# Optimization experiments

Hardware: AMD Instinct MI355X
Metric: run time of the kernel (lower is better)

Reference implementation:

```python
import jax, jax.numpy as jnp
import numpy as np

N, E, C_IN, HID, G, L = 100000, 1600000, 64, 32, 128, 3
NEG_SLOPE = 0.01  # F.leaky_relu default


def setup_inputs() -> dict:
    key = jax.random.key(0)
    ks = jax.random.split(key, 10)
    x = jax.random.normal(ks[0], (N, C_IN), dtype=jnp.float32)
    src = jax.random.randint(ks[1], (E,), 0, N, dtype=jnp.int32)
    dst = jax.random.randint(ks[2], (E,), 0, N, dtype=jnp.int32)
    batch = jnp.sort(jax.random.randint(ks[3], (N,), 0, G, dtype=jnp.int32))
    def glorot(k, fan_in, fan_out):
        lim = np.sqrt(6.0 / (fan_in + fan_out)).astype(np.float32)
        return jax.random.uniform(k, (fan_in, fan_out), jnp.float32, -lim, lim)
    W0 = glorot(ks[4], C_IN, HID); b0 = jnp.zeros((HID,), jnp.float32)
    W1 = glorot(ks[5], HID, HID);  b1 = jnp.zeros((HID,), jnp.float32)
    W2 = glorot(ks[6], HID, HID);  b2 = jnp.zeros((HID,), jnp.float32)
    return {"x": x, "W0": W0, "b0": b0, "W1": W1, "b1": b1,
            "W2": W2, "b2": b2, "src": src, "dst": dst, "batch": batch}


def _gcn_conv(x, W, b, src, dst, dinv):
    # PyG GCNConv: h = x W; aggregate with sym-norm (A + I)
    h = x @ W                                   # [N, H]
    coef = (dinv[src] * dinv[dst])[:, None]     # [E, 1]
    msg = h[src] * coef                         # gather + scale
    agg = jax.ops.segment_sum(msg, dst, num_segments=N)
    agg = agg + h * (dinv * dinv)[:, None]      # self-loop term
    return agg + b


def _mean_pool(x, batch, counts):
    s = jax.ops.segment_sum(x, batch, num_segments=G)
    return s / counts[:, None]


def reference(x, W0, b0, W1, b1, W2, b2, src, dst, batch):
    # degree with self loops (edge weight 1), as PyG gcn_norm does
    deg = jax.ops.segment_sum(jnp.ones((E,), x.dtype), dst, num_segments=N) + 1.0
    dinv = jax.lax.rsqrt(deg)
    counts = jnp.maximum(
        jax.ops.segment_sum(jnp.ones((N,), x.dtype), batch, num_segments=G), 1.0)
    params = [(W0, b0), (W1, b1), (W2, b2)]
    feats = []
    h = x
    for W, b in params:
        h = _gcn_conv(h, W, b, src, dst, dinv)
        h = jax.nn.leaky_relu(h, NEG_SLOPE)
        feats.append(_mean_pool(h, batch, counts))
    merge = jnp.mean(jnp.stack(feats, axis=0), axis=0)  # [G, HID]
    return merge
```

## Files before the change

kernel.cpp:

```cpp
#include <hip/hip_runtime.h>
#include <hip/hip_bf16.h>

#define NN 100000
#define NE 1600000
#define CIN 64
#define HIDN 32
#define NG 128
#define SLOPE 0.01f


__global__ __launch_bounds__(256) void k_rank(const int* __restrict__ dst,
                                              int* __restrict__ deg,
                                              int* __restrict__ rank,
                                              int qbase, int qcount) {
  int i0 = blockIdx.x * 256 + threadIdx.x;
  if (i0 >= qcount) return;
  int i = qbase + i0;
  int4 d = ((const int4*)dst)[i];
  int4 r;
  r.x = atomicAdd(&deg[d.x], 1);
  r.y = atomicAdd(&deg[d.y], 1);
  r.z = atomicAdd(&deg[d.z], 1);
  r.w = atomicAdd(&deg[d.w], 1);
  ((int4*)rank)[i] = r;
}


__global__ __launch_bounds__(256) void k_scan1(const int* __restrict__ deg,
                                               int* __restrict__ bsum) {
  __shared__ int s[256];
  int t = threadIdx.x;
  int base = blockIdx.x * 1024 + t * 4;
  int sum = 0;
#pragma unroll
  for (int j = 0; j < 4; ++j) {
    int idx = base + j;
    if (idx < NN) sum += deg[idx];
  }
  s[t] = sum;
  __syncthreads();
  for (int o = 128; o > 0; o >>= 1) {
    if (t < o) s[t] += s[t + o];
    __syncthreads();
  }
  if (t == 0) bsum[blockIdx.x] = s[0];
}

__global__ __launch_bounds__(256) void k_mid(int* __restrict__ bsum,
                                             int* __restrict__ rowp,
                                             const int* __restrict__ batch,
                                             float* __restrict__ cinv, int nblk) {
  __shared__ int s[128];
  __shared__ int sb[NG + 1];
  int t = threadIdx.x;
  if (t < nblk) s[t] = bsum[t];
  if (t <= NG) {
    int lo = 0, hi = NN;
    while (lo < hi) {
      int mid = (lo + hi) >> 1;
      if (batch[mid] < t) lo = mid + 1; else hi = mid;
    }
    sb[t] = lo;
  }
  __syncthreads();
  if (t == 0) {
    int run = 0;
    for (int i = 0; i < nblk; ++i) {
      int v = s[i];
      s[i] = run;
      run += v;
    }
    rowp[NN] = run;
  }
  __syncthreads();
  if (t < nblk) bsum[t] = s[t];
  if (t < NG) {
    int c = sb[t + 1] - sb[t];
    cinv[t] = 1.0f / (3.0f * fmaxf((float)c, 1.0f));
  }
}

__global__ __launch_bounds__(256) void k_scan3(const int* __restrict__ deg,
                                               const int* __restrict__ bsum,
                                               int* __restrict__ rowp,
                                               float* __restrict__ dinv) {
  __shared__ int s[256];
  int t = threadIdx.x;
  int base = blockIdx.x * 1024 + t * 4;
  int d0 = 0, d1 = 0, d2 = 0, d3 = 0;
  if (base < NN) d0 = deg[base];
  if (base + 1 < NN) d1 = deg[base + 1];
  if (base + 2 < NN) d2 = deg[base + 2];
  if (base + 3 < NN) d3 = deg[base + 3];
  int ts = d0 + d1 + d2 + d3;
  s[t] = ts;
  __syncthreads();
  for (int o = 1; o < 256; o <<= 1) {
    int v = (t >= o) ? s[t - o] : 0;
    __syncthreads();
    s[t] += v;
    __syncthreads();
  }
  int run = bsum[blockIdx.x] + s[t] - ts;
  if (base < NN) { rowp[base] = run; dinv[base] = rsqrtf((float)d0 + 1.0f); run += d0; }
  if (base + 1 < NN) { rowp[base + 1] = run; dinv[base + 1] = rsqrtf((float)d1 + 1.0f); run += d1; }
  if (base + 2 < NN) { rowp[base + 2] = run; dinv[base + 2] = rsqrtf((float)d2 + 1.0f); run += d2; }
  if (base + 3 < NN) { rowp[base + 3] = run; dinv[base + 3] = rsqrtf((float)d3 + 1.0f); run += d3; }
}

__global__ __launch_bounds__(256) void k_scatter(const int* __restrict__ src,
                                                 const int* __restrict__ dst,
                                                 const int* __restrict__ rank,
                                                 const int* __restrict__ rowp,
                                                 int* __restrict__ col,
                                                 int qbase, int qcount) {
  int i0 = blockIdx.x * 256 + threadIdx.x;
  if (i0 >= qcount) return;
  int i = qbase + i0;
  int4 d = ((const int4*)dst)[i];
  int4 r = ((const int4*)rank)[i];
  int4 s = ((const int4*)src)[i];
  col[rowp[d.x] + r.x] = s.x;
  col[rowp[d.y] + r.y] = s.y;
  col[rowp[d.z] + r.z] = s.z;
  col[rowp[d.w] + r.w] = s.w;
}


template <int K>
__global__ __launch_bounds__(256) void k_mm(const float* __restrict__ in,
                                            const float* __restrict__ W,
                                            const float* __restrict__ dinv,
                                            __hip_bfloat16* __restrict__ out) {
  __shared__ float sW[K * HIDN];
  int t = threadIdx.x;
  for (int i = t; i < K * HIDN; i += 256) sW[i] = W[i];
  __syncthreads();
  int gid = blockIdx.x * 256 + t;
  int node = gid >> 5;
  int f = gid & 31;
  if (node >= NN) return;
  const float* xr = in + node * K;
  float acc = 0.f;
#pragma unroll
  for (int k = 0; k < K; ++k) acc += xr[k] * sW[k * HIDN + f];
  out[node * HIDN + f] = __float2bfloat16(acc * dinv[node]);
}


template <int WRITE_H>
__global__ __launch_bounds__(256) void k_agg(const __hip_bfloat16* __restrict__ hs,
                                             const int* __restrict__ rowp,
                                             const int* __restrict__ col,
                                             const float* __restrict__ dinv,
                                             const int* __restrict__ batch,
                                             const float* __restrict__ cinv,
                                             const float* __restrict__ bias,
                                             float* __restrict__ hout,
                                             float* __restrict__ pool) {
  const int t = threadIdx.x;
  const int f = t & 31;
  const int sub = t >> 5;
  const float bf = bias[f];
  float pacc = 0.f;
  int gcur = -1;
  const int base = blockIdx.x * 32;
#pragma unroll
  for (int it = 0; it < 4; ++it) {
    const int i = base + it * 8 + sub;
    if (i < NN) {
      float acc = __bfloat162float(hs[i * HIDN + f]);
      const int rs = rowp[i];
      const int re = rowp[i + 1];
      int e = rs;
      for (; e + 8 <= re; e += 8) {
        const int c0 = __builtin_nontemporal_load(col + e);
        const int c1 = __builtin_nontemporal_load(col + e + 1);
        const int c2 = __builtin_nontemporal_load(col + e + 2);
        const int c3 = __builtin_nontemporal_load(col + e + 3);
        const int c4 = __builtin_nontemporal_load(col + e + 4);
        const int c5 = __builtin_nontemporal_load(col + e + 5);
        const int c6 = __builtin_nontemporal_load(col + e + 6);
        const int c7 = __builtin_nontemporal_load(col + e + 7);
        const float v0 = __bfloat162float(hs[c0 * HIDN + f]);
        const float v1 = __bfloat162float(hs[c1 * HIDN + f]);
        const float v2 = __bfloat162float(hs[c2 * HIDN + f]);
        const float v3 = __bfloat162float(hs[c3 * HIDN + f]);
        const float v4 = __bfloat162float(hs[c4 * HIDN + f]);
        const float v5 = __bfloat162float(hs[c5 * HIDN + f]);
        const float v6 = __bfloat162float(hs[c6 * HIDN + f]);
        const float v7 = __bfloat162float(hs[c7 * HIDN + f]);
        acc += ((v0 + v1) + (v2 + v3)) + ((v4 + v5) + (v6 + v7));
      }
      for (; e + 4 <= re; e += 4) {
        const int c0 = __builtin_nontemporal_load(col + e);
        const int c1 = __builtin_nontemporal_load(col + e + 1);
        const int c2 = __builtin_nontemporal_load(col + e + 2);
        const int c3 = __builtin_nontemporal_load(col + e + 3);
        const float v0 = __bfloat162float(hs[c0 * HIDN + f]);
        const float v1 = __bfloat162float(hs[c1 * HIDN + f]);
        const float v2 = __bfloat162float(hs[c2 * HIDN + f]);
        const float v3 = __bfloat162float(hs[c3 * HIDN + f]);
        acc += (v0 + v1) + (v2 + v3);
      }
      for (; e < re; ++e) acc += __bfloat162float(hs[col[e] * HIDN + f]);
      float v = acc * dinv[i] + bf;
      v = v > 0.f ? v : SLOPE * v;
      if (WRITE_H) hout[i * HIDN + f] = v;
      const int g = batch[i];
      if (g != gcur) {
        if (gcur >= 0) unsafeAtomicAdd(&pool[gcur * HIDN + f], pacc * cinv[gcur]);
        gcur = g;
        pacc = 0.f;
      }
      pacc += v;
    }
  }
  if (gcur >= 0) unsafeAtomicAdd(&pool[gcur * HIDN + f], pacc * cinv[gcur]);
}


extern "C" void kernel_launch(void* const* d_in, const int* in_sizes, int n_in,
                              void* d_out, int out_size, void* d_ws, size_t ws_size,
                              hipStream_t stream) {
  const float* x = (const float*)d_in[0];
  const float* W0 = (const float*)d_in[1];
  const float* b0 = (const float*)d_in[2];
  const float* W1 = (const float*)d_in[3];
  const float* b1 = (const float*)d_in[4];
  const float* W2 = (const float*)d_in[5];
  const float* b2 = (const float*)d_in[6];
  const int* src = (const int*)d_in[7];
  const int* dst = (const int*)d_in[8];
  const int* batch = (const int*)d_in[9];
  float* out = (float*)d_out;

  char* ws = (char*)d_ws;
  auto carve = [&](size_t bytes) -> char* {
    char* p = ws;
    ws += (bytes + 255) & ~(size_t)255;
    return p;
  };
  int* deg = (int*)carve(NN * 4);
  int* rank = (int*)carve((size_t)NE * 4);
  int* rowp = (int*)carve((NN + 1) * 4);
  int* bsum = (int*)carve(128 * 4);
  float* dinv = (float*)carve(NN * 4);
  float* cinv = (float*)carve(NG * 4);
  int* col = (int*)carve((size_t)NE * 4);
  float* hA = (float*)carve((size_t)NN * HIDN * 4);
  __hip_bfloat16* hs = (__hip_bfloat16*)carve((size_t)NN * HIDN * 2);

  hipMemsetAsync(deg, 0, NN * 4, stream);
  hipMemsetAsync(out, 0, NG * HIDN * 4, stream);

  const int QH = NE / 4 / 2;
  const int half_grid = (QH + 255) / 256;
  k_rank<<<half_grid, 256, 0, stream>>>(dst, deg, rank, 0, QH);
  k_rank<<<half_grid, 256, 0, stream>>>(dst, deg, rank, QH, QH);

  int nblk = (NN + 1023) / 1024;
  k_scan1<<<nblk, 256, 0, stream>>>(deg, bsum);
  k_mid<<<1, 256, 0, stream>>>(bsum, rowp, batch, cinv, nblk);
  k_scan3<<<nblk, 256, 0, stream>>>(deg, bsum, rowp, dinv);

  k_scatter<<<half_grid, 256, 0, stream>>>(src, dst, rank, rowp, col, 0, QH);
  k_scatter<<<half_grid, 256, 0, stream>>>(src, dst, rank, rowp, col, QH, QH);

  const int mm_grid = (NN * HIDN + 255) / 256;
  const int agg_grid = (NN + 31) / 32;

  k_mm<CIN><<<mm_grid, 256, 0, stream>>>(x, W0, dinv, hs);
  k_agg<1><<<agg_grid, 256, 0, stream>>>(hs, rowp, col, dinv, batch, cinv, b0, hA, out);
  k_mm<HIDN><<<mm_grid, 256, 0, stream>>>(hA, W1, dinv, hs);
  k_agg<1><<<agg_grid, 256, 0, stream>>>(hs, rowp, col, dinv, batch, cinv, b1, hA, out);
  k_mm<HIDN><<<mm_grid, 256, 0, stream>>>(hA, W2, dinv, hs);
  k_agg<0><<<agg_grid, 256, 0, stream>>>(hs, rowp, col, dinv, batch, cinv, b2, hA, out);
}
```

Baseline: 473.6 us.

## Balance edge work across warps in aggregation and pack edge ranks into bytes

The aggregation kernel now splits each 32-node block's edge range evenly across its 8 warps, not one node per warp. Each warp accumulates per-row partial sums into shared memory with atomics, and the epilogue then applies self-loop, bias, activation and pooling. Edge ranks are packed as 8-bit values, four per word, which cuts rank traffic. The rank and scatter kernels are merged into single launches handling 8 edges per thread, and the output memset is folded into k_mid. The packing assumes every in-degree is below 256, and the grid assumes NN divisible by 32, so both depend on this input shape.

```diff
diff --git a/kernel.cpp b/kernel.cpp
--- a/kernel.cpp
+++ b/kernel.cpp
@@ -11,18 +11,23 @@
 
 __global__ __launch_bounds__(256) void k_rank(const int* __restrict__ dst,
                                               int* __restrict__ deg,
-                                              int* __restrict__ rank,
-                                              int qbase, int qcount) {
-  int i0 = blockIdx.x * 256 + threadIdx.x;
-  if (i0 >= qcount) return;
-  int i = qbase + i0;
-  int4 d = ((const int4*)dst)[i];
-  int4 r;
-  r.x = atomicAdd(&deg[d.x], 1);
-  r.y = atomicAdd(&deg[d.y], 1);
-  r.z = atomicAdd(&deg[d.z], 1);
-  r.w = atomicAdd(&deg[d.w], 1);
-  ((int4*)rank)[i] = r;
+                                              unsigned int* __restrict__ rank) {
+  int i = blockIdx.x * 256 + threadIdx.x;
+  if (i * 8 >= NE) return;
+  int4 a = ((const int4*)dst)[2 * i];
+  int4 b = ((const int4*)dst)[2 * i + 1];
+  unsigned int r0 = atomicAdd(&deg[a.x], 1);
+  unsigned int r1 = atomicAdd(&deg[a.y], 1);
+  unsigned int r2 = atomicAdd(&deg[a.z], 1);
+  unsigned int r3 = atomicAdd(&deg[a.w], 1);
+  unsigned int r4 = atomicAdd(&deg[b.x], 1);
+  unsigned int r5 = atomicAdd(&deg[b.y], 1);
+  unsigned int r6 = atomicAdd(&deg[b.z], 1);
+  unsigned int r7 = atomicAdd(&deg[b.w], 1);
+  uint2 packed;
+  packed.x = r0 | (r1 << 8) | (r2 << 16) | (r3 << 24);
+  packed.y = r4 | (r5 << 8) | (r6 << 16) | (r7 << 24);
+  ((uint2*)rank)[i] = packed;
 }
 
 
@@ -49,7 +54,8 @@
 __global__ __launch_bounds__(256) void k_mid(int* __restrict__ bsum,
                                              int* __restrict__ rowp,
                                              const int* __restrict__ batch,
-                                             float* __restrict__ cinv, int nblk) {
+                                             float* __restrict__ cinv,
+                                             float* __restrict__ out, int nblk) {
   __shared__ int s[128];
   __shared__ int sb[NG + 1];
   int t = threadIdx.x;
@@ -62,6 +68,7 @@
     }
     sb[t] = lo;
   }
+  for (int i = t; i < NG * HIDN; i += 256) out[i] = 0.f;
   __syncthreads();
   if (t == 0) {
     int run = 0;
@@ -110,20 +117,26 @@
 
 __global__ __launch_bounds__(256) void k_scatter(const int* __restrict__ src,
                                                  const int* __restrict__ dst,
-                                                 const int* __restrict__ rank,
+                                                 const unsigned int* __restrict__ rank,
                                                  const int* __restrict__ rowp,
-                                                 int* __restrict__ col,
-                                                 int qbase, int qcount) {
-  int i0 = blockIdx.x * 256 + threadIdx.x;
-  if (i0 >= qcount) return;
-  int i = qbase + i0;
-  int4 d = ((const int4*)dst)[i];
-  int4 r = ((const int4*)rank)[i];
-  int4 s = ((const int4*)src)[i];
-  col[rowp[d.x] + r.x] = s.x;
-  col[rowp[d.y] + r.y] = s.y;
-  col[rowp[d.z] + r.z] = s.z;
-  col[rowp[d.w] + r.w] = s.w;
+                                                 int* __restrict__ col) {
+  int i = blockIdx.x * 256 + threadIdx.x;
+  if (i * 8 >= NE) return;
+  int4 da = ((const int4*)dst)[2 * i];
+  int4 db = ((const int4*)dst)[2 * i + 1];
+  uint2 rr = ((const uint2*)rank)[i];
+  int4 sa = ((const int4*)src)[2 * i];
+  int4 sb = ((const int4*)src)[2 * i + 1];
+  int p0 = rowp[da.x] + (int)(rr.x & 0xff);
+  int p1 = rowp[da.y] + (int)((rr.x >> 8) & 0xff);
+  int p2 = rowp[da.z] + (int)((rr.x >> 16) & 0xff);
+  int p3 = rowp[da.w] + (int)(rr.x >> 24);
+  int p4 = rowp[db.x] + (int)(rr.y & 0xff);
+  int p5 = rowp[db.y] + (int)((rr.y >> 8) & 0xff);
+  int p6 = rowp[db.z] + (int)((rr.y >> 16) & 0xff);
+  int p7 = rowp[db.w] + (int)(rr.y >> 24);
+  col[p0] = sa.x; col[p1] = sa.y; col[p2] = sa.z; col[p3] = sa.w;
+  col[p4] = sb.x; col[p5] = sb.y; col[p6] = sb.z; col[p7] = sb.w;
 }
 
 
@@ -158,63 +171,78 @@
                                              const float* __restrict__ bias,
                                              float* __restrict__ hout,
                                              float* __restrict__ pool) {
+  __shared__ float part[32][32];
+  __shared__ int srow[33];
   const int t = threadIdx.x;
   const int f = t & 31;
   const int sub = t >> 5;
+  const int base = blockIdx.x * 32;
+
+  ((float4*)part)[t] = float4{0.f, 0.f, 0.f, 0.f};
+  if (t < 33) srow[t] = rowp[base + t];
+  __syncthreads();
+
+  const int rs0 = srow[0];
+  const int T = srow[32] - rs0;
+  int e = rs0 + (T * sub) / 8;
+  const int eE = rs0 + (T * (sub + 1)) / 8;
+
+  int j;
+  {
+    int lo = 0, hi = 32;
+    while (lo < hi) {
+      int mid = (lo + hi) >> 1;
+      if (srow[mid + 1] <= e) lo = mid + 1; else hi = mid;
+    }
+    j = lo;
+  }
+
+  float acc = 0.f;
+  while (e < eE) {
+    const int rend = srow[j + 1];
+    const int nb = rend < eE ? rend : eE;
+    while (nb - e >= 8) {
+      const int c0 = col[e], c1 = col[e + 1], c2 = col[e + 2], c3 = col[e + 3];
+      const int c4 = col[e + 4], c5 = col[e + 5], c6 = col[e + 6], c7 = col[e + 7];
+      const float v0 = __bfloat162float(hs[c0 * HIDN + f]);
+      const float v1 = __bfloat162float(hs[c1 * HIDN + f]);
+      const float v2 = __bfloat162float(hs[c2 * HIDN + f]);
+      const float v3 = __bfloat162float(hs[c3 * HIDN + f]);
+      const float v4 = __bfloat162float(hs[c4 * HIDN + f]);
+      const float v5 = __bfloat162float(hs[c5 * HIDN + f]);
+      const float v6 = __bfloat162float(hs[c6 * HIDN + f]);
+      const float v7 = __bfloat162float(hs[c7 * HIDN + f]);
+      acc += ((v0 + v1) + (v2 + v3)) + ((v4 + v5) + (v6 + v7));
+      e += 8;
+    }
+    while (e < nb) {
+      acc += __bfloat162float(hs[col[e] * HIDN + f]);
+      ++e;
+    }
+    atomicAdd(&part[j][f], acc);
+    acc = 0.f;
+    if (nb == rend) ++j;
+  }
+  __syncthreads();
+
   const float bf = bias[f];
   float pacc = 0.f;
   int gcur = -1;
-  const int base = blockIdx.x * 32;
 #pragma unroll
-  for (int it = 0; it < 4; ++it) {
-    const int i = base + it * 8 + sub;
-    if (i < NN) {
-      float acc = __bfloat162float(hs[i * HIDN + f]);
-      const int rs = rowp[i];
-      const int re = rowp[i + 1];
-      int e = rs;
-      for (; e + 8 <= re; e += 8) {
-        const int c0 = __builtin_nontemporal_load(col + e);
-        const int c1 = __builtin_nontemporal_load(col + e + 1);
-        const int c2 = __builtin_nontemporal_load(col + e + 2);
-        const int c3 = __builtin_nontemporal_load(col + e + 3);
-        const int c4 = __builtin_nontemporal_load(col + e + 4);
-        const int c5 = __builtin_nontemporal_load(col + e + 5);
-        const int c6 = __builtin_nontemporal_load(col + e + 6);
-        const int c7 = __builtin_nontemporal_load(col + e + 7);
-        const float v0 = __bfloat162float(hs[c0 * HIDN + f]);
-        const float v1 = __bfloat162float(hs[c1 * HIDN + f]);
-        const float v2 = __bfloat162float(hs[c2 * HIDN + f]);
-        const float v3 = __bfloat162float(hs[c3 * HIDN + f]);
-        const float v4 = __bfloat162float(hs[c4 * HIDN + f]);
-        const float v5 = __bfloat162float(hs[c5 * HIDN + f]);
-        const float v6 = __bfloat162float(hs[c6 * HIDN + f]);
-        const float v7 = __bfloat162float(hs[c7 * HIDN + f]);
-        acc += ((v0 + v1) + (v2 + v3)) + ((v4 + v5) + (v6 + v7));
-      }
-      for (; e + 4 <= re; e += 4) {
-        const int c0 = __builtin_nontemporal_load(col + e);
-        const int c1 = __builtin_nontemporal_load(col + e + 1);
-        const int c2 = __builtin_nontemporal_load(col + e + 2);
-        const int c3 = __builtin_nontemporal_load(col + e + 3);
-        const float v0 = __bfloat162float(hs[c0 * HIDN + f]);
-        const float v1 = __bfloat162float(hs[c1 * HIDN + f]);
-        const float v2 = __bfloat162float(hs[c2 * HIDN + f]);
-        const float v3 = __bfloat162float(hs[c3 * HIDN + f]);
-        acc += (v0 + v1) + (v2 + v3);
-      }
-      for (; e < re; ++e) acc += __bfloat162float(hs[col[e] * HIDN + f]);
-      float v = acc * dinv[i] + bf;
-      v = v > 0.f ? v : SLOPE * v;
-      if (WRITE_H) hout[i * HIDN + f] = v;
-      const int g = batch[i];
-      if (g != gcur) {
-        if (gcur >= 0) unsafeAtomicAdd(&pool[gcur * HIDN + f], pacc * cinv[gcur]);
-        gcur = g;
-        pacc = 0.f;
-      }
-      pacc += v;
-    }
+  for (int q = 0; q < 4; ++q) {
+    const int li = sub * 4 + q;
+    const int i = base + li;
+    const float self = __bfloat162float(hs[i * HIDN + f]);
+    float v = (part[li][f] + self) * dinv[i] + bf;
+    v = v > 0.f ? v : SLOPE * v;
+    if (WRITE_H) hout[i * HIDN + f] = v;
+    const int g = batch[i];
+    if (g != gcur) {
+      if (gcur >= 0) unsafeAtomicAdd(&pool[gcur * HIDN + f], pacc * cinv[gcur]);
+      gcur = g;
+      pacc = 0.f;
+    }
+    pacc += v;
   }
   if (gcur >= 0) unsafeAtomicAdd(&pool[gcur * HIDN + f], pacc * cinv[gcur]);
 }
@@ -242,7 +270,7 @@
     return p;
   };
   int* deg = (int*)carve(NN * 4);
-  int* rank = (int*)carve((size_t)NE * 4);
+  unsigned int* rank = (unsigned int*)carve((size_t)NE);
   int* rowp = (int*)carve((NN + 1) * 4);
   int* bsum = (int*)carve(128 * 4);
   float* dinv = (float*)carve(NN * 4);
@@ -252,23 +280,19 @@
   __hip_bfloat16* hs = (__hip_bfloat16*)carve((size_t)NN * HIDN * 2);
 
   hipMemsetAsync(deg, 0, NN * 4, stream);
-  hipMemsetAsync(out, 0, NG * HIDN * 4, stream);
-
-  const int QH = NE / 4 / 2;
-  const int half_grid = (QH + 255) / 256;
-  k_rank<<<half_grid, 256, 0, stream>>>(dst, deg, rank, 0, QH);
-  k_rank<<<half_grid, 256, 0, stream>>>(dst, deg, rank, QH, QH);
+
+  const int oct_grid = (NE / 8 + 255) / 256;
+  k_rank<<<oct_grid, 256, 0, stream>>>(dst, deg, rank);
 
   int nblk = (NN + 1023) / 1024;
   k_scan1<<<nblk, 256, 0, stream>>>(deg, bsum);
-  k_mid<<<1, 256, 0, stream>>>(bsum, rowp, batch, cinv, nblk);
+  k_mid<<<1, 256, 0, stream>>>(bsum, rowp, batch, cinv, out, nblk);
   k_scan3<<<nblk, 256, 0, stream>>>(deg, bsum, rowp, dinv);
 
-  k_scatter<<<half_grid, 256, 0, stream>>>(src, dst, rank, rowp, col, 0, QH);
-  k_scatter<<<half_grid, 256, 0, stream>>>(src, dst, rank, rowp, col, QH, QH);
+  k_scatter<<<oct_grid, 256, 0, stream>>>(src, dst, rank, rowp, col);
 
   const int mm_grid = (NN * HIDN + 255) / 256;
-  const int agg_grid = (NN + 31) / 32;
+  const int agg_grid = NN / 32;
 
   k_mm<CIN><<<mm_grid, 256, 0, stream>>>(x, W0, dinv, hs);
   k_agg<1><<<agg_grid, 256, 0, stream>>>(hs, rowp, col, dinv, batch, cinv, b0, hA, out);
```

Measured after the change: 498.7 us. 1.05x slower.
